# Optimization experiments

Hardware: AMD Instinct MI355X
Metric: run time of the kernel (lower is better)

The kernel has to match this reference:

```python
import jax, jax.numpy as jnp
import numpy as np

B, S, D_IN = 2, 2048, 1024
DIM, H, G = 64, 16, 4  # head dim, num_heads, kv groups


def setup_inputs() -> dict:
    key = jax.random.key(0)
    ks = jax.random.split(key, 9)
    query = jax.random.normal(ks[0], (B, S, D_IN), dtype=jnp.float32)
    key_t = jax.random.normal(ks[1], (B, S, D_IN), dtype=jnp.float32)
    value = jax.random.normal(ks[2], (B, S, D_IN), dtype=jnp.float32)
    # causal mask; masked_fill where mask == 0
    mask = jnp.tril(jnp.ones((S, S), dtype=jnp.int32))[None]  # [1,S,S]
    sc = 1.0 / np.sqrt(D_IN)
    Wq = jax.random.normal(ks[3], (H, D_IN, DIM), dtype=jnp.float32) * sc
    bq = jnp.zeros((H, DIM), dtype=jnp.float32)
    Wk = jax.random.normal(ks[4], (G, D_IN, DIM), dtype=jnp.float32) * sc
    bk = jnp.zeros((G, DIM), dtype=jnp.float32)
    Wv = jax.random.normal(ks[5], (G, D_IN, DIM), dtype=jnp.float32) * sc
    bv = jnp.zeros((G, DIM), dtype=jnp.float32)
    return {"query": query, "key": key_t, "value": value, "mask": mask,
            "Wq": Wq, "bq": bq, "Wk": Wk, "bk": bk, "Wv": Wv, "bv": bv}


def reference(query, key, value, mask, Wq, bq, Wk, bk, Wv, bv):
    # batched per-head projections (replaces the Python loop over heads)
    Q = jnp.einsum('bsd,hde->bhse', query, Wq) + bq[None, :, None, :]   # [B,H,S,E]
    K = jnp.einsum('bsd,gde->bgse', key, Wk) + bk[None, :, None, :]     # [B,G,S,E]
    V = jnp.einsum('bsd,gde->bgse', value, Wv) + bv[None, :, None, :]   # [B,G,S,E]
    # head i uses KV group i % G (as in the original loop)
    g_idx = jnp.arange(H) % G
    Kh = K[:, g_idx]  # [B,H,S,E]
    Vh = V[:, g_idx]
    attn = jnp.einsum('bhqe,bhke->bhqk', Q, Kh) / np.sqrt(DIM)          # [B,H,S,S]
    attn = jnp.where(mask[:, None] == 0, jnp.float32(-1e9), attn)
    p = jax.nn.softmax(attn, axis=-1)
    z = jnp.einsum('bhqk,bhke->bhqe', p, Vh)                             # [B,H,S,E]
    # concat heads along last dim (same order as torch.cat of z_list)
    return z.transpose(0, 2, 1, 3).reshape(B, S, H * DIM)
```

## Files before the change

kernel.cpp:

```cpp
#include <hip/hip_runtime.h>
#include <hip/hip_bf16.h>
#include <math.h>

#define S_LEN 2048
#define DIN   1024
#define NH    16
#define NG    4

typedef short s16x8 __attribute__((ext_vector_type(8)));
typedef float f32x4 __attribute__((ext_vector_type(4)));

__device__ __forceinline__ unsigned short f2bf(float x) {
  union { float f; unsigned u; } v; v.f = x;
  unsigned r = v.u + 0x7FFFu + ((v.u >> 16) & 1u);
  return (unsigned short)(r >> 16);
}
__device__ __forceinline__ unsigned cvtpk(float a, float b) {
  unsigned r;
  asm("v_cvt_pk_bf16_f32 %0, %1, %2" : "=v"(r) : "v"(a), "v"(b));
  return r;
}


__global__ __launch_bounds__(256) void k_cast(
    const float* __restrict__ q, const float* __restrict__ k,
    const float* __restrict__ v, unsigned short* __restrict__ AF) {
  const float* src = (blockIdx.y == 0) ? q : (blockIdx.y == 1) ? k : v;
  unsigned short* dst = AF + (size_t)blockIdx.y * 4194304;
  int flat = blockIdx.x * 256 + threadIdx.x;
  int b = flat >> 18, s = (flat >> 7) & 2047, d0 = (flat & 127) * 8;
  const float* sp = src + (size_t)(b * 2048 + s) * 1024 + d0;
  float4 x = *(const float4*)sp;
  float4 y = *(const float4*)(sp + 4);
  union { s16x8 v; unsigned u[4]; } r;
  r.u[0] = cvtpk(x.x, x.y); r.u[1] = cvtpk(x.z, x.w);
  r.u[2] = cvtpk(y.x, y.y); r.u[3] = cvtpk(y.z, y.w);
  unsigned short* p = dst + (size_t)((b * 128 + (s >> 4)) * 32 + (d0 >> 5)) * 512
                    + (s & 15) * 8 + ((d0 >> 3) & 3) * 128;
  *(s16x8*)p = r.v;
}

__global__ __launch_bounds__(256) void k_wtrans(
    const float* __restrict__ Wq, const float* __restrict__ Wk,
    const float* __restrict__ Wv, unsigned short* __restrict__ WF) {
  __shared__ __align__(16) unsigned short T[64][72];
  const int u = blockIdx.x >> 4, D0 = (blockIdx.x & 15) * 64;
  const int t = threadIdx.x;
  const float* src = (u < 16) ? (Wq + (size_t)u * 65536)
                   : (u < 20) ? (Wk + (size_t)(u - 16) * 65536)
                              : (Wv + (size_t)(u - 20) * 65536);
  const int e4 = (t & 15) * 4, dl = t >> 4;
  #pragma unroll
  for (int p = 0; p < 4; ++p) {
    const int d = p * 16 + dl;
    float4 v = *(const float4*)(src + (size_t)(D0 + d) * 64 + e4);
    T[e4 + 0][d] = f2bf(v.x); T[e4 + 1][d] = f2bf(v.y);
    T[e4 + 2][d] = f2bf(v.z); T[e4 + 3][d] = f2bf(v.w);
  }
  __syncthreads();
  const int j = t & 7;
  #pragma unroll
  for (int p = 0; p < 2; ++p) {
    const int e = p * 32 + (t >> 3);
    unsigned short* dst = WF + (size_t)u * 65536
        + (size_t)((e >> 4) * 32 + (D0 >> 5) + (j >> 2)) * 512
        + (e & 15) * 8 + (j & 3) * 128;
    *(s16x8*)dst = *(const s16x8*)&T[e][j * 8];
  }
}

__global__ __launch_bounds__(256, 2) void k_project(
    const unsigned short* __restrict__ AF,
    const float* __restrict__ bq, const float* __restrict__ bk,
    const float* __restrict__ bv,
    const unsigned short* __restrict__ WF,
    unsigned short* __restrict__ QF,
    unsigned short* __restrict__ KF,
    unsigned short* __restrict__ VF) {
  const int i = blockIdx.x;
  const int lid = (i & 7) * 96 + (i >> 3);
  const int strip = lid / 48;
  const int rr = lid % 48;
  const int b = rr / 24, u = rr % 24;
  const int tid = threadIdx.x;
  const int w = tid >> 6, lane = tid & 63, lq = lane & 15, gq = lane >> 4;

  const unsigned short* AFp = AF
      + (size_t)((u < 16) ? 0 : (u < 20) ? 1 : 2) * 4194304
      + (size_t)b * 2097152;
  const float* bias = (u < 16) ? bq + u * 64
                    : (u < 20) ? bk + (u - 16) * 64 : bv + (u - 20) * 64;
  const unsigned short* WFp = WF + (size_t)u * 65536;
  const int sb0 = strip * 8 + w * 2;
  const float OSC = (u < 16) ? 0.1803368801111204f : 1.0f;

  f32x4 acc[2][4] = {};
  #pragma unroll 2
  for (int dk = 0; dk < 32; ++dk) {
    s16x8 a[2], bf[4];
    #pragma unroll
    for (int rf = 0; rf < 2; ++rf)
      a[rf] = *(const s16x8*)(AFp + (size_t)((sb0 + rf) * 32 + dk) * 512 + lane * 8);
    #pragma unroll
    for (int n = 0; n < 4; ++n)
      bf[n] = *(const s16x8*)(WFp + (size_t)(n * 32 + dk) * 512 + lane * 8);
    #pragma unroll
    for (int rf = 0; rf < 2; ++rf)
      #pragma unroll
      for (int n = 0; n < 4; ++n)
        acc[rf][n] = __builtin_amdgcn_mfma_f32_16x16x32_bf16(a[rf], bf[n], acc[rf][n], 0, 0, 0);
  }

  float bvv[4];
  #pragma unroll
  for (int n = 0; n < 4; ++n) bvv[n] = bias[n * 16 + lq];

  unsigned short* dst = (u < 16) ? QF + (size_t)(b * 16 + u) * 131072
                      : (u < 20) ? KF + (size_t)(b * 4 + (u - 16)) * 131072
                                 : VF + (size_t)(b * 4 + (u - 20)) * 131072;
  #pragma unroll
  for (int rf = 0; rf < 2; ++rf)
    #pragma unroll
    for (int n = 0; n < 4; ++n)
      #pragma unroll
      for (int r = 0; r < 4; ++r) {
        const int s = strip * 128 + w * 32 + rf * 16 + gq * 4 + r;
        const int d = n * 16 + lq;
        const unsigned short hv = f2bf((acc[rf][n][r] + bvv[n]) * OSC);
        if (u < 20)
          dst[(size_t)((s >> 4) * 2 + (d >> 5)) * 512
              + (s & 15) * 8 + ((d >> 3) & 3) * 128 + (d & 7)] = hv;
        else
          dst[(size_t)(n * 64 + (s >> 5)) * 512
              + lq * 8 + ((s >> 3) & 3) * 128 + (s & 7)] = hv;
      }
}

__global__ __launch_bounds__(256, 3) void k_attn(
    const unsigned short* __restrict__ QF, const unsigned short* __restrict__ KF,
    const unsigned short* __restrict__ VF, float* __restrict__ out) {
  __shared__ __align__(16) unsigned short P[4][16][72];
  const int tid = threadIdx.x;
  const int w = tid >> 6, lane = tid & 63, lq = lane & 15, gq = lane >> 4;
  const int x = blockIdx.x;
  const int xcd = x & 7, li = x >> 3;
  const int g = xcd & 3;
  const int j = 127 - (li * 2 + (xcd >> 2));
  const int h = g + 4 * w;
  const int b = blockIdx.y;

  const unsigned short* QFp = QF + (size_t)(b * NH + h) * 131072;
  const unsigned short* KFp = KF + (size_t)(b * NG + g) * 131072;
  const unsigned short* VFp = VF + (size_t)(b * NG + g) * 131072;
  const int nt = (j >> 2) + 1;

  const s16x8 qf0 = *(const s16x8*)(QFp + (size_t)(j * 2 + 0) * 512 + lane * 8);
  const s16x8 qf1 = *(const s16x8*)(QFp + (size_t)(j * 2 + 1) * 512 + lane * 8);
  f32x4 z[4] = {};
  float lsum = 0.f;

  auto loadK = [&](s16x8 (&A)[4], s16x8 (&B)[4], int t) {
    #pragma unroll
    for (int f = 0; f < 4; ++f) {
      const unsigned short* kp = KFp + (size_t)((t * 4 + f) * 2) * 512 + lane * 8;
      A[f] = *(const s16x8*)kp;
      B[f] = *(const s16x8*)(kp + 512);
    }
  };

  auto tile = [&](const s16x8 (&kA)[4], const s16x8 (&kB)[4], int t) {
    const int k0 = t * 64;
    s16x8 vb[4][2];
    #pragma unroll
    for (int n = 0; n < 4; ++n)
      #pragma unroll
      for (int ks = 0; ks < 2; ++ks)
        vb[n][ks] = *(const s16x8*)(VFp + (size_t)(n * 64 + t * 2 + ks) * 512 + lane * 8);
    f32x4 sv[4];
    __builtin_amdgcn_s_setprio(1);
    #pragma unroll
    for (int f = 0; f < 4; ++f) {
      f32x4 s = {};
      s = __builtin_amdgcn_mfma_f32_16x16x32_bf16(kA[f], qf0, s, 0, 0, 0);
      s = __builtin_amdgcn_mfma_f32_16x16x32_bf16(kB[f], qf1, s, 0, 0, 0);
      sv[f] = s;
    }
    __builtin_amdgcn_s_setprio(0);
    if (t == nt - 1) {
      const int qrow = j * 16 + lq;
      #pragma unroll
      for (int f = 0; f < 4; ++f)
        #pragma unroll
        for (int r = 0; r < 4; ++r)
          if (k0 + f * 16 + gq * 4 + r > qrow) sv[f][r] = -1e30f;
    }
    float s0 = 0.f, s1 = 0.f;
    #pragma unroll
    for (int f = 0; f < 4; ++f) {
      float p0 = __builtin_amdgcn_exp2f(sv[f][0]);
      float p1 = __builtin_amdgcn_exp2f(sv[f][1]);
      float p2 = __builtin_amdgcn_exp2f(sv[f][2]);
      float p3 = __builtin_amdgcn_exp2f(sv[f][3]);
      s0 += p0 + p1; s1 += p2 + p3;
      *(uint2*)&P[w][lq][f * 16 + gq * 4] = make_uint2(cvtpk(p0, p1), cvtpk(p2, p3));
    }
    lsum += s0 + s1;
    s16x8 pa[2];
    #pragma unroll
    for (int ks = 0; ks < 2; ++ks)
      pa[ks] = *(const s16x8*)&P[w][lq][ks * 32 + gq * 8];
    __builtin_amdgcn_s_setprio(1);
    #pragma unroll
    for (int n = 0; n < 4; ++n)
      #pragma unroll
      for (int ks = 0; ks < 2; ++ks)
        z[n] = __builtin_amdgcn_mfma_f32_16x16x32_bf16(pa[ks], vb[n][ks], z[n], 0, 0, 0);
    __builtin_amdgcn_s_setprio(0);
  };

  s16x8 cA[4], cB[4], nA[4], nB[4];
  loadK(cA, cB, 0);
  int t = 0;
  while (true) {
    loadK(nA, nB, (t + 1 < nt) ? t + 1 : t);
    tile(cA, cB, t);
    if (++t >= nt) break;
    loadK(cA, cB, (t + 1 < nt) ? t + 1 : t);
    tile(nA, nB, t);
    if (++t >= nt) break;
  }

  lsum += __shfl_xor(lsum, 16);
  lsum += __shfl_xor(lsum, 32);
  float* outp = out + (size_t)b * S_LEN * 1024 + h * 64;
  #pragma unroll
  for (int r = 0; r < 4; ++r) {
    float lr = __shfl(lsum, gq * 4 + r, 64);
    float inv = __builtin_amdgcn_rcpf(lr);
    float* op = outp + (size_t)(j * 16 + gq * 4 + r) * 1024;
    #pragma unroll
    for (int n = 0; n < 4; ++n) op[n * 16 + lq] = z[n][r] * inv;
  }
}

extern "C" void kernel_launch(void* const* d_in, const int* in_sizes, int n_in,
                              void* d_out, int out_size, void* d_ws, size_t ws_size,
                              hipStream_t stream) {
  const float* query = (const float*)d_in[0];
  const float* key   = (const float*)d_in[1];
  const float* value = (const float*)d_in[2];
  const float* Wq = (const float*)d_in[4];
  const float* bq = (const float*)d_in[5];
  const float* Wk = (const float*)d_in[6];
  const float* bk = (const float*)d_in[7];
  const float* Wv = (const float*)d_in[8];
  const float* bv = (const float*)d_in[9];
  float* out = (float*)d_out;

  unsigned short* AF = (unsigned short*)d_ws;
  unsigned short* WF = AF + 12582912;
  unsigned short* QF = WF + 1572864;
  unsigned short* KF = QF + 4194304;
  unsigned short* VF = KF + 1048576;

  hipLaunchKernelGGL(k_cast, dim3(2048, 3), dim3(256), 0, stream,
                     query, key, value, AF);
  hipLaunchKernelGGL(k_wtrans, dim3(384), dim3(256), 0, stream, Wq, Wk, Wv, WF);
  hipLaunchKernelGGL(k_project, dim3(768), dim3(256), 0, stream,
                     AF, bq, bk, bv, WF, QF, KF, VF);
  hipLaunchKernelGGL(k_attn, dim3(512, 2), dim3(256), 0, stream, QF, KF, VF, out);
}
```

Baseline: 91.44 us.

## Fuse fp32-to-bf16 input cast into projection kernel via LDS staging

Removes the separate cast kernel and its bf16 workspace. Each projection block now loads a 32-row fp32 strip of query, key or value, converts it to bf16 into LDS in MFMA fragment layout, and reuses it across all heads or groups for that input. This cuts a full write and reread of the bf16 activations and one launch. In exchange the grid drops to 384 blocks, and each wave loops serially over 8 or 2 heads with unbalanced work: Q blocks do 4x the work of K/V blocks. Weight tiles are streamed from global memory with less reuse per load.

```diff
diff --git a/kernel.cpp b/kernel.cpp
--- a/kernel.cpp
+++ b/kernel.cpp
@@ -20,25 +20,13 @@
   asm("v_cvt_pk_bf16_f32 %0, %1, %2" : "=v"(r) : "v"(a), "v"(b));
   return r;
 }
-
-
-__global__ __launch_bounds__(256) void k_cast(
-    const float* __restrict__ q, const float* __restrict__ k,
-    const float* __restrict__ v, unsigned short* __restrict__ AF) {
-  const float* src = (blockIdx.y == 0) ? q : (blockIdx.y == 1) ? k : v;
-  unsigned short* dst = AF + (size_t)blockIdx.y * 4194304;
-  int flat = blockIdx.x * 256 + threadIdx.x;
-  int b = flat >> 18, s = (flat >> 7) & 2047, d0 = (flat & 127) * 8;
-  const float* sp = src + (size_t)(b * 2048 + s) * 1024 + d0;
-  float4 x = *(const float4*)sp;
-  float4 y = *(const float4*)(sp + 4);
+__device__ __forceinline__ s16x8 cvt8(float4 a, float4 b) {
   union { s16x8 v; unsigned u[4]; } r;
-  r.u[0] = cvtpk(x.x, x.y); r.u[1] = cvtpk(x.z, x.w);
-  r.u[2] = cvtpk(y.x, y.y); r.u[3] = cvtpk(y.z, y.w);
-  unsigned short* p = dst + (size_t)((b * 128 + (s >> 4)) * 32 + (d0 >> 5)) * 512
-                    + (s & 15) * 8 + ((d0 >> 3) & 3) * 128;
-  *(s16x8*)p = r.v;
-}
+  r.u[0] = cvtpk(a.x, a.y); r.u[1] = cvtpk(a.z, a.w);
+  r.u[2] = cvtpk(b.x, b.y); r.u[3] = cvtpk(b.z, b.w);
+  return r.v;
+}
+
 
 __global__ __launch_bounds__(256) void k_wtrans(
     const float* __restrict__ Wq, const float* __restrict__ Wk,
@@ -69,71 +57,77 @@
   }
 }
 
-__global__ __launch_bounds__(256, 2) void k_project(
-    const unsigned short* __restrict__ AF,
+__global__ __launch_bounds__(256) void k_proj_fused(
+    const float* __restrict__ query, const float* __restrict__ key,
+    const float* __restrict__ value,
     const float* __restrict__ bq, const float* __restrict__ bk,
     const float* __restrict__ bv,
     const unsigned short* __restrict__ WF,
     unsigned short* __restrict__ QF,
     unsigned short* __restrict__ KF,
     unsigned short* __restrict__ VF) {
-  const int i = blockIdx.x;
-  const int lid = (i & 7) * 96 + (i >> 3);
-  const int strip = lid / 48;
-  const int rr = lid % 48;
-  const int b = rr / 24, u = rr % 24;
-  const int tid = threadIdx.x;
-  const int w = tid >> 6, lane = tid & 63, lq = lane & 15, gq = lane >> 4;
-
-  const unsigned short* AFp = AF
-      + (size_t)((u < 16) ? 0 : (u < 20) ? 1 : 2) * 4194304
-      + (size_t)b * 2097152;
-  const float* bias = (u < 16) ? bq + u * 64
-                    : (u < 20) ? bk + (u - 16) * 64 : bv + (u - 20) * 64;
-  const unsigned short* WFp = WF + (size_t)u * 65536;
-  const int sb0 = strip * 8 + w * 2;
-  const float OSC = (u < 16) ? 0.1803368801111204f : 1.0f;
-
-  f32x4 acc[2][4] = {};
-  #pragma unroll 2
-  for (int dk = 0; dk < 32; ++dk) {
-    s16x8 a[2], bf[4];
-    #pragma unroll
-    for (int rf = 0; rf < 2; ++rf)
-      a[rf] = *(const s16x8*)(AFp + (size_t)((sb0 + rf) * 32 + dk) * 512 + lane * 8);
+  __shared__ __align__(16) unsigned short AT[2][32][512];
+  const int x = blockIdx.x;
+  const int i = x >> 7;
+  const int r = x & 127;
+  const int b = r >> 6, strip = r & 63;
+  const int t = threadIdx.x;
+
+  const float* src = ((i == 0) ? query : (i == 1) ? key : value)
+                   + ((size_t)b * S_LEN + strip * 32) * DIN;
+  #pragma unroll 4
+  for (int c = 0; c < 16; ++c) {
+    const int idx = c * 2048 + t * 8;
+    const int row = idx >> 10, d = idx & 1023;
+    const float* sp = src + (size_t)row * DIN + d;
+    float4 xv = *(const float4*)sp;
+    float4 yv = *(const float4*)(sp + 4);
+    *(s16x8*)&AT[row >> 4][d >> 5][(row & 15) * 8 + ((d >> 3) & 3) * 128] =
+        cvt8(xv, yv);
+  }
+  __syncthreads();
+
+  const int w = t >> 6, lane = t & 63, lq = lane & 15, gq = lane >> 4;
+  const int rt = w & 1, uh = w >> 1;
+  const int cnt = (i == 0) ? 8 : 2;
+  const int u0 = uh * cnt;
+  const float* bias0 = (i == 0) ? bq : (i == 1) ? bk : bv;
+  const float OSC = (i == 0) ? 0.1803368801111204f : 1.0f;
+
+  for (int u = u0; u < u0 + cnt; ++u) {
+    const int ug = (i == 0) ? u : (i == 1) ? 16 + u : 20 + u;
+    const unsigned short* WFp = WF + (size_t)ug * 65536;
+    f32x4 acc[4] = {};
+    for (int kt = 0; kt < 32; ++kt) {
+      const s16x8 a = *(const s16x8*)&AT[rt][kt][lane * 8];
+      #pragma unroll
+      for (int n = 0; n < 4; ++n) {
+        const s16x8 bf = *(const s16x8*)(WFp + (size_t)(n * 32 + kt) * 512 + lane * 8);
+        acc[n] = __builtin_amdgcn_mfma_f32_16x16x32_bf16(a, bf, acc[n], 0, 0, 0);
+      }
+    }
+    float bvv[4];
+    #pragma unroll
+    for (int n = 0; n < 4; ++n) bvv[n] = bias0[u * 64 + n * 16 + lq];
+
+    unsigned short* dst = (i == 0) ? QF + (size_t)(b * 16 + u) * 131072
+                        : (i == 1) ? KF + (size_t)(b * 4 + u) * 131072
+                                   : VF + (size_t)(b * 4 + u) * 131072;
     #pragma unroll
     for (int n = 0; n < 4; ++n)
-      bf[n] = *(const s16x8*)(WFp + (size_t)(n * 32 + dk) * 512 + lane * 8);
-    #pragma unroll
-    for (int rf = 0; rf < 2; ++rf)
-      #pragma unroll
-      for (int n = 0; n < 4; ++n)
-        acc[rf][n] = __builtin_amdgcn_mfma_f32_16x16x32_bf16(a[rf], bf[n], acc[rf][n], 0, 0, 0);
-  }
-
-  float bvv[4];
-  #pragma unroll
-  for (int n = 0; n < 4; ++n) bvv[n] = bias[n * 16 + lq];
-
-  unsigned short* dst = (u < 16) ? QF + (size_t)(b * 16 + u) * 131072
-                      : (u < 20) ? KF + (size_t)(b * 4 + (u - 16)) * 131072
-                                 : VF + (size_t)(b * 4 + (u - 20)) * 131072;
-  #pragma unroll
-  for (int rf = 0; rf < 2; ++rf)
-    #pragma unroll
-    for (int n = 0; n < 4; ++n)
-      #pragma unroll
-      for (int r = 0; r < 4; ++r) {
-        const int s = strip * 128 + w * 32 + rf * 16 + gq * 4 + r;
+      #pragma unroll
+      for (int rr = 0; rr < 4; ++rr) {
+        const int s = strip * 32 + rt * 16 + gq * 4 + rr;
         const int d = n * 16 + lq;
-        const unsigned short hv = f2bf((acc[rf][n][r] + bvv[n]) * OSC);
-        if (u < 20)
+        const unsigned short hv = f2bf((acc[n][rr] + bvv[n]) * OSC);
+        if (i < 2)
           dst[(size_t)((s >> 4) * 2 + (d >> 5)) * 512
               + (s & 15) * 8 + ((d >> 3) & 3) * 128 + (d & 7)] = hv;
         else
           dst[(size_t)(n * 64 + (s >> 5)) * 512
               + lq * 8 + ((s >> 3) & 3) * 128 + (s & 7)] = hv;
       }
+  }
 }
 
 __global__ __launch_bounds__(256, 3) void k_attn(
@@ -257,16 +251,13 @@
   const float* bv = (const float*)d_in[9];
   float* out = (float*)d_out;
 
-  unsigned short* AF = (unsigned short*)d_ws;
-  unsigned short* WF = AF + 12582912;
+  unsigned short* WF = (unsigned short*)d_ws;
   unsigned short* QF = WF + 1572864;
   unsigned short* KF = QF + 4194304;
   unsigned short* VF = KF + 1048576;
 
-  hipLaunchKernelGGL(k_cast, dim3(2048, 3), dim3(256), 0, stream,
-                     query, key, value, AF);
   hipLaunchKernelGGL(k_wtrans, dim3(384), dim3(256), 0, stream, Wq, Wk, Wv, WF);
-  hipLaunchKernelGGL(k_project, dim3(768), dim3(256), 0, stream,
-                     AF, bq, bk, bv, WF, QF, KF, VF);
+  hipLaunchKernelGGL(k_proj_fused, dim3(384), dim3(256), 0, stream,
+                     query, key, value, bq, bk, bv, WF, QF, KF, VF);
   hipLaunchKernelGGL(k_attn, dim3(512, 2), dim3(256), 0, stream, QF, KF, VF, out);
 }
```

New measurement: 172.1 us. 88.2% more time.
